# Performance work log

Measured on AMD Instinct MI355X. Metric: run time of the kernel, lower is better.

The kernel has to match this reference:

```python
import jax, jax.numpy as jnp
import numpy as np

D_MODEL = 768
NUM_HEADS = 12
HEAD_DIM = D_MODEL // NUM_HEADS
SEQ = 4096
BATCH = 1


def setup_inputs() -> dict:
    key = jax.random.key(0)
    ks = jax.random.split(key, 6)
    scale = 1.0 / np.sqrt(D_MODEL)
    x = jax.random.normal(ks[0], (BATCH, SEQ, D_MODEL), dtype=jnp.float32)
    mask = jnp.tril(jnp.ones((SEQ, SEQ), dtype=bool))[None, None]  # [1,1,S,S] causal
    Wq = jax.random.normal(ks[1], (D_MODEL, D_MODEL), dtype=jnp.float32) * scale
    Wk = jax.random.normal(ks[2], (D_MODEL, D_MODEL), dtype=jnp.float32) * scale
    Wv = jax.random.normal(ks[3], (D_MODEL, D_MODEL), dtype=jnp.float32) * scale
    Wo = jax.random.normal(ks[4], (D_MODEL, D_MODEL), dtype=jnp.float32) * scale
    bo = jax.random.normal(ks[5], (D_MODEL,), dtype=jnp.float32) * 0.01
    return {"x": x, "mask": mask, "Wq": Wq, "Wk": Wk, "Wv": Wv, "Wo": Wo, "bo": bo}


def _rope_tables(seq_len, head_dim, dtype):
    # inv_freq over even dims; emb = cat(freqs, freqs) but only the first half
    # participates in the well-defined rotation (x1/x2 have head_dim//2 channels)
    inv_freq = 1.0 / (10000.0 ** (jnp.arange(0, head_dim, 2, dtype=dtype) / head_dim))
    t = jnp.arange(seq_len, dtype=dtype)
    freqs = t[:, None] * inv_freq[None, :]  # [S, head_dim//2]
    return jnp.cos(freqs), jnp.sin(freqs)


def _apply_rotary(xh, cos, sin):
    # xh: [B,H,S,hd]; cos/sin: [S, hd//2]
    x1 = xh[..., ::2]
    x2 = xh[..., 1::2]
    # faithful to source: concatenated (not interleaved) rotated halves
    return jnp.concatenate([x1 * cos - x2 * sin, x1 * sin + x2 * cos], axis=-1)


def reference(x, mask, Wq, Wk, Wv, Wo, bo):
    B, S, D = x.shape
    H, hd = NUM_HEADS, HEAD_DIM
    def split_heads(y):
        return y.reshape(B, S, H, hd).transpose(0, 2, 1, 3)  # [B,H,S,hd]
    q = split_heads(x @ Wq.T)
    k = split_heads(x @ Wk.T)
    v = split_heads(x @ Wv.T)
    cos, sin = _rope_tables(S, hd, x.dtype)
    q = _apply_rotary(q, cos, sin)
    k = _apply_rotary(k, cos, sin)
    scores = jnp.einsum('bhqd,bhkd->bhqk', q, k) / jnp.sqrt(jnp.asarray(hd, x.dtype))
    scores = jnp.where(mask, scores, jnp.asarray(-1e9, x.dtype))
    attn = jax.nn.softmax(scores, axis=-1)  # dropout is identity in eval
    out = jnp.einsum('bhqk,bhkd->bhqd', attn, v)
    out = out.transpose(0, 2, 1, 3).reshape(B, S, D)
    return out @ Wo.T + bo
```

## Files before the change

kernel.cpp:

```cpp
#include <hip/hip_runtime.h>
#include <hip/hip_bf16.h>
#include <math.h>

#define SEQ 4096
#define DM  768
#define NH  12
#define HD  64
#define PER ((size_t)NH * SEQ * HD)
#define XN  ((size_t)SEQ * DM)
#define WN  ((size_t)DM * DM)

typedef __attribute__((ext_vector_type(8))) short bf16x8;
typedef __attribute__((ext_vector_type(4))) short s16x4;
typedef __attribute__((ext_vector_type(4))) float f32x4;

#define MFMA(a, b, c) __builtin_amdgcn_mfma_f32_16x16x32_bf16((a), (b), (c), 0, 0, 0)

#if __has_builtin(__builtin_amdgcn_exp2f)
#define EXP2(x) __builtin_amdgcn_exp2f(x)
#else
#define EXP2(x) exp2f(x)
#endif

#define SWZ(row, blk) (((row) << 6) + ((((blk) ^ ((row) & 7))) << 3))

__device__ __forceinline__ unsigned short f2b(float f) {
    unsigned int u = __float_as_uint(f);
    u += 0x7FFFu + ((u >> 16) & 1u);
    return (unsigned short)(u >> 16);
}

__global__ __launch_bounds__(256) void cvt_kernel(const float* __restrict__ src,
                                                  unsigned short* __restrict__ dst,
                                                  int n4) {
    for (int i = blockIdx.x * 256 + threadIdx.x; i < n4; i += gridDim.x * 256) {
        const float4 v = ((const float4*)src)[i];
        s16x4 p;
        p.x = (short)f2b(v.x); p.y = (short)f2b(v.y);
        p.z = (short)f2b(v.z); p.w = (short)f2b(v.w);
        ((s16x4*)dst)[i] = p;
    }
}

__global__ __launch_bounds__(256) void rope_kernel(float2* __restrict__ rope) {
    const int g = blockIdx.x * 256 + threadIdx.x;
    const int row = g >> 5, fi = g & 31;
    const float invf = expf(-(float)fi * 0.28782313662425576f);
    float sn, cs;
    sincosf((float)row * invf, &sn, &cs);
    rope[row * 32 + fi] = make_float2(cs, sn);
}

__global__ __launch_bounds__(256) void qkv_mfma(
    const float* __restrict__ x,  const unsigned short* __restrict__ xb,
    const float* __restrict__ Wq, const float* __restrict__ Wk, const float* __restrict__ Wv,
    const unsigned short* __restrict__ Wqb, const unsigned short* __restrict__ Wkb,
    const unsigned short* __restrict__ Wvb,
    const float2* __restrict__ rope,
    unsigned short* __restrict__ Qo, unsigned short* __restrict__ Ko,
    unsigned short* __restrict__ Vo, int fast)
{
    __shared__ __align__(16) unsigned short Xs[2][4096];
    __shared__ __align__(16) unsigned short Ws[2][4096];
    __shared__ unsigned short VL[64 * 66];

    const int t    = threadIdx.x;
    const int w    = t >> 6;
    const int lane = t & 63;
    const int quad = lane >> 4;
    const int l16  = lane & 15;

    const int nt_b = blockIdx.y;
    const float* W; const unsigned short* Wb; int region;
    if (nt_b < 12)      { W = Wq; Wb = Wqb; region = 0; }
    else if (nt_b < 24) { W = Wk; Wb = Wkb; region = 1; }
    else                { W = Wv; Wb = Wvb; region = 2; }
    const int h  = nt_b % 12;
    const int s0 = blockIdx.x * 64;
    const int n0 = h * 64;

    f32x4 acc[4] = {{0,0,0,0},{0,0,0,0},{0,0,0,0},{0,0,0,0}};
    const int prow = t >> 3, pblk = t & 7;

    bf16x8 xr0, xr1, wr0, wr1;
    if (fast) {
        xr0 = *(const bf16x8*)&xb[(size_t)(s0 + prow) * DM + pblk * 8];
        xr1 = *(const bf16x8*)&xb[(size_t)(s0 + prow + 32) * DM + pblk * 8];
        wr0 = *(const bf16x8*)&Wb[(size_t)(n0 + prow) * DM + pblk * 8];
        wr1 = *(const bf16x8*)&Wb[(size_t)(n0 + prow + 32) * DM + pblk * 8];
        *(bf16x8*)&Xs[0][SWZ(prow, pblk)]      = xr0;
        *(bf16x8*)&Xs[0][SWZ(prow + 32, pblk)] = xr1;
        *(bf16x8*)&Ws[0][SWZ(prow, pblk)]      = wr0;
        *(bf16x8*)&Ws[0][SWZ(prow + 32, pblk)] = wr1;
    } else {
        for (int e = t; e < 1024; e += 256) {
            const int row = e >> 4, c4 = e & 15;
            const int off = SWZ(row, c4 >> 1) + (c4 & 1) * 4;
            const float4 xv = *(const float4*)&x[(size_t)(s0 + row) * DM + c4 * 4];
            s16x4 px; px.x = (short)f2b(xv.x); px.y = (short)f2b(xv.y);
            px.z = (short)f2b(xv.z); px.w = (short)f2b(xv.w);
            *(s16x4*)&Xs[0][off] = px;
            const float4 wv = *(const float4*)&W[(size_t)(n0 + row) * DM + c4 * 4];
            s16x4 pw; pw.x = (short)f2b(wv.x); pw.y = (short)f2b(wv.y);
            pw.z = (short)f2b(wv.z); pw.w = (short)f2b(wv.w);
            *(s16x4*)&Ws[0][off] = pw;
        }
    }
    __syncthreads();

    for (int kt = 0; kt < 12; ++kt) {
        const unsigned short* Xb  = Xs[kt & 1];
        const unsigned short* Wbt = Ws[kt & 1];
        if (fast && kt < 11) {
            const int k0 = (kt + 1) * 64;
            xr0 = *(const bf16x8*)&xb[(size_t)(s0 + prow) * DM + k0 + pblk * 8];
            xr1 = *(const bf16x8*)&xb[(size_t)(s0 + prow + 32) * DM + k0 + pblk * 8];
            wr0 = *(const bf16x8*)&Wb[(size_t)(n0 + prow) * DM + k0 + pblk * 8];
            wr1 = *(const bf16x8*)&Wb[(size_t)(n0 + prow + 32) * DM + k0 + pblk * 8];
        }
        const bf16x8 a0 = *(const bf16x8*)&Xb[SWZ(16 * w + l16, quad)];
        const bf16x8 a1 = *(const bf16x8*)&Xb[SWZ(16 * w + l16, 4 + quad)];
        #pragma unroll
        for (int nt = 0; nt < 4; ++nt) {
            const bf16x8 b0 = *(const bf16x8*)&Wbt[SWZ(16 * nt + l16, quad)];
            const bf16x8 b1 = *(const bf16x8*)&Wbt[SWZ(16 * nt + l16, 4 + quad)];
            acc[nt] = MFMA(a0, b0, acc[nt]);
            acc[nt] = MFMA(a1, b1, acc[nt]);
        }
        if (kt < 11) {
            const int nb = (kt + 1) & 1;
            if (fast) {
                *(bf16x8*)&Xs[nb][SWZ(prow, pblk)]      = xr0;
                *(bf16x8*)&Xs[nb][SWZ(prow + 32, pblk)] = xr1;
                *(bf16x8*)&Ws[nb][SWZ(prow, pblk)]      = wr0;
                *(bf16x8*)&Ws[nb][SWZ(prow + 32, pblk)] = wr1;
            } else {
                const int k0 = (kt + 1) * 64;
                for (int e = t; e < 1024; e += 256) {
                    const int row = e >> 4, c4 = e & 15;
                    const int off = SWZ(row, c4 >> 1) + (c4 & 1) * 4;
                    const float4 xv = *(const float4*)&x[(size_t)(s0 + row) * DM + k0 + c4 * 4];
                    s16x4 px; px.x = (short)f2b(xv.x); px.y = (short)f2b(xv.y);
                    px.z = (short)f2b(xv.z); px.w = (short)f2b(xv.w);
                    *(s16x4*)&Xs[nb][off] = px;
                    const float4 wv = *(const float4*)&W[(size_t)(n0 + row) * DM + k0 + c4 * 4];
                    s16x4 pw; pw.x = (short)f2b(wv.x); pw.y = (short)f2b(wv.y);
                    pw.z = (short)f2b(wv.z); pw.w = (short)f2b(wv.w);
                    *(s16x4*)&Ws[nb][off] = pw;
                }
            }
        }
        __syncthreads();
    }

    const size_t headoff = (size_t)h * SEQ * HD;
    if (region <= 1) {
        unsigned short* dst = (region == 0) ? Qo : Ko;
        const float qsc = (region == 0) ? 0.18033688011112042f : 1.0f;
        #pragma unroll
        for (int nt = 0; nt < 4; ++nt)
            #pragma unroll
            for (int r = 0; r < 4; ++r) {
                const int srow = s0 + 16 * w + quad * 4 + r;
                const int d  = nt * 16 + l16;
                const int fi = d >> 1;
                const float own = acc[nt][r] * qsc;
                const float oth = __shfl_xor(own, 1);
                float cs, sn;
                if (fast) {
                    const float2 t2 = rope[srow * 32 + fi];
                    cs = t2.x; sn = t2.y;
                } else {
                    const float invf = expf(-(float)fi * 0.28782313662425576f);
                    sincosf((float)srow * invf, &sn, &cs);
                }
                const float val = (d & 1) ? (oth * sn + own * cs)
                                          : (own * cs - oth * sn);
                dst[headoff + (size_t)srow * HD + ((d & 1) ? 32 : 0) + fi] = f2b(val);
            }
    } else {
        #pragma unroll
        for (int nt = 0; nt < 4; ++nt)
            #pragma unroll
            for (int r = 0; r < 4; ++r)
                VL[(nt * 16 + l16) * 66 + 16 * w + quad * 4 + r] = f2b(acc[nt][r]);
        __syncthreads();
        for (int e = t; e < 2048; e += 256) {
            const int d = e >> 5, sp = e & 31;
            const unsigned int v = (unsigned int)VL[d * 66 + 2 * sp] |
                                   ((unsigned int)VL[d * 66 + 2 * sp + 1] << 16);
            *(unsigned int*)&Vo[headoff + (size_t)d * SEQ + s0 + 2 * sp] = v;
        }
    }
}

__global__ __launch_bounds__(256) void attn_mfma(
    const unsigned short* __restrict__ Q,
    const unsigned short* __restrict__ K,
    const unsigned short* __restrict__ V,
    unsigned short* __restrict__ O)
{
    __shared__ unsigned short Kst[2][4096];
    __shared__ unsigned short Vt [2][4096];
    __shared__ unsigned short Ps [4096];

    const int h    = blockIdx.y;
    const int q0   = (63 - blockIdx.x) * 64;
    const int t    = threadIdx.x;
    const int w    = t >> 6;
    const int lane = t & 63;
    const int quad = lane >> 4;
    const int l16  = lane & 15;
    const size_t headoff = (size_t)h * SEQ * HD;

    for (int e = t; e < 512; e += 256) {
        const int row = e >> 3, blk = e & 7;
        *(bf16x8*)&Ps[SWZ(row, blk)] =
            *(const bf16x8*)&Q[headoff + (size_t)(q0 + row) * HD + blk * 8];
    }
    const int prow = t >> 3, pblk = t & 7;
    bf16x8 kr0 = *(const bf16x8*)&K[headoff + (size_t)prow * HD + pblk * 8];
    bf16x8 kr1 = *(const bf16x8*)&K[headoff + (size_t)(prow + 32) * HD + pblk * 8];
    bf16x8 vr0 = *(const bf16x8*)&V[headoff + (size_t)prow * SEQ + pblk * 8];
    bf16x8 vr1 = *(const bf16x8*)&V[headoff + (size_t)(prow + 32) * SEQ + pblk * 8];
    *(bf16x8*)&Kst[0][SWZ(prow, pblk)]      = kr0;
    *(bf16x8*)&Kst[0][SWZ(prow + 32, pblk)] = kr1;
    *(bf16x8*)&Vt[0][SWZ(prow, pblk)]       = vr0;
    *(bf16x8*)&Vt[0][SWZ(prow + 32, pblk)]  = vr1;
    __syncthreads();

    const bf16x8 aQ0 = *(const bf16x8*)&Ps[SWZ(16 * w + l16, quad)];
    const bf16x8 aQ1 = *(const bf16x8*)&Ps[SWZ(16 * w + l16, 4 + quad)];

    bf16x8 ones;
    #pragma unroll
    for (int i = 0; i < 8; ++i) ones[i] = (short)0x3F80;

    f32x4 oA[4] = {{0,0,0,0},{0,0,0,0},{0,0,0,0},{0,0,0,0}};
    f32x4 lA = {0, 0, 0, 0};
    const int cmax = q0 >> 6;

    for (int c = 0; c <= cmax; ++c) {
        const unsigned short* Kb = Kst[c & 1];
        const unsigned short* Vb = Vt[c & 1];
        if (c < cmax) {
            const int kn = (c + 1) * 64;
            kr0 = *(const bf16x8*)&K[headoff + (size_t)(kn + prow) * HD + pblk * 8];
            kr1 = *(const bf16x8*)&K[headoff + (size_t)(kn + prow + 32) * HD + pblk * 8];
            vr0 = *(const bf16x8*)&V[headoff + (size_t)prow * SEQ + kn + pblk * 8];
            vr1 = *(const bf16x8*)&V[headoff + (size_t)(prow + 32) * SEQ + kn + pblk * 8];
        }

        f32x4 sA[4] = {{0,0,0,0},{0,0,0,0},{0,0,0,0},{0,0,0,0}};
        #pragma unroll
        for (int nt = 0; nt < 4; ++nt) {
            const bf16x8 b0 = *(const bf16x8*)&Kb[SWZ(16 * nt + l16, quad)];
            const bf16x8 b1 = *(const bf16x8*)&Kb[SWZ(16 * nt + l16, 4 + quad)];
            sA[nt] = MFMA(aQ0, b0, sA[nt]);
            sA[nt] = MFMA(aQ1, b1, sA[nt]);
        }

        if (c == cmax) {
            #pragma unroll
            for (int nt = 0; nt < 4; ++nt) {
                const int key = nt * 16 + l16;
                #pragma unroll
                for (int r = 0; r < 4; ++r) {
                    const int qrel = 16 * w + quad * 4 + r;
                    if (key > qrel) sA[nt][r] = -1e30f;
                }
            }
        }

        #pragma unroll
        for (int nt = 0; nt < 4; ++nt)
            #pragma unroll
            for (int r = 0; r < 4; ++r)
                Ps[SWZ(16 * w + quad * 4 + r, 2 * nt + (l16 >> 3)) + (l16 & 7)] =
                    f2b(EXP2(sA[nt][r]));
        asm volatile("s_waitcnt lgkmcnt(0)" ::: "memory");
        const bf16x8 aP0 = *(const bf16x8*)&Ps[SWZ(16 * w + l16, quad)];
        const bf16x8 aP1 = *(const bf16x8*)&Ps[SWZ(16 * w + l16, 4 + quad)];

        #pragma unroll
        for (int nt = 0; nt < 4; ++nt) {
            const bf16x8 v0 = *(const bf16x8*)&Vb[SWZ(16 * nt + l16, quad)];
            const bf16x8 v1 = *(const bf16x8*)&Vb[SWZ(16 * nt + l16, 4 + quad)];
            oA[nt] = MFMA(aP0, v0, oA[nt]);
            oA[nt] = MFMA(aP1, v1, oA[nt]);
        }
        lA = MFMA(aP0, ones, lA);
        lA = MFMA(aP1, ones, lA);

        if (c < cmax) {
            const int nb = (c + 1) & 1;
            *(bf16x8*)&Kst[nb][SWZ(prow, pblk)]      = kr0;
            *(bf16x8*)&Kst[nb][SWZ(prow + 32, pblk)] = kr1;
            *(bf16x8*)&Vt[nb][SWZ(prow, pblk)]       = vr0;
            *(bf16x8*)&Vt[nb][SWZ(prow + 32, pblk)]  = vr1;
        }
        __syncthreads();
    }

    float inv[4];
    #pragma unroll
    for (int r = 0; r < 4; ++r) inv[r] = 1.0f / lA[r];
    #pragma unroll
    for (int nt = 0; nt < 4; ++nt)
        #pragma unroll
        for (int r = 0; r < 4; ++r) {
            const int q = q0 + 16 * w + quad * 4 + r;
            O[(size_t)q * DM + h * HD + nt * 16 + l16] = f2b(oA[nt][r] * inv[r]);
        }
}

__global__ __launch_bounds__(256) void proj_mfma(
    const unsigned short* __restrict__ A,
    const float* __restrict__ Wo, const unsigned short* __restrict__ Wob,
    const float* __restrict__ bo,
    float* __restrict__ out, int fast)
{
    __shared__ __align__(16) unsigned short Xs[2][4096];
    __shared__ __align__(16) unsigned short Ws[2][4096];

    const int t    = threadIdx.x;
    const int w    = t >> 6;
    const int lane = t & 63;
    const int quad = lane >> 4;
    const int l16  = lane & 15;
    const int s0 = blockIdx.x * 64;
    const int n0 = blockIdx.y * 64;
    const int prow = t >> 3, pblk = t & 7;

    f32x4 acc[4] = {{0,0,0,0},{0,0,0,0},{0,0,0,0},{0,0,0,0}};

    bf16x8 ar0, ar1, wr0, wr1;
    ar0 = *(const bf16x8*)&A[(size_t)(s0 + prow) * DM + pblk * 8];
    ar1 = *(const bf16x8*)&A[(size_t)(s0 + prow + 32) * DM + pblk * 8];
    *(bf16x8*)&Xs[0][SWZ(prow, pblk)]      = ar0;
    *(bf16x8*)&Xs[0][SWZ(prow + 32, pblk)] = ar1;
    if (fast) {
        wr0 = *(const bf16x8*)&Wob[(size_t)(n0 + prow) * DM + pblk * 8];
        wr1 = *(const bf16x8*)&Wob[(size_t)(n0 + prow + 32) * DM + pblk * 8];
        *(bf16x8*)&Ws[0][SWZ(prow, pblk)]      = wr0;
        *(bf16x8*)&Ws[0][SWZ(prow + 32, pblk)] = wr1;
    } else {
        for (int e = t; e < 1024; e += 256) {
            const int row = e >> 4, c4 = e & 15;
            const float4 wv = *(const float4*)&Wo[(size_t)(n0 + row) * DM + c4 * 4];
            s16x4 pw; pw.x = (short)f2b(wv.x); pw.y = (short)f2b(wv.y);
            pw.z = (short)f2b(wv.z); pw.w = (short)f2b(wv.w);
            *(s16x4*)&Ws[0][SWZ(row, c4 >> 1) + (c4 & 1) * 4] = pw;
        }
    }
    __syncthreads();

    for (int kt = 0; kt < 12; ++kt) {
        const unsigned short* Xb  = Xs[kt & 1];
        const unsigned short* Wbt = Ws[kt & 1];
        if (kt < 11) {
            const int k0 = (kt + 1) * 64;
            ar0 = *(const bf16x8*)&A[(size_t)(s0 + prow) * DM + k0 + pblk * 8];
            ar1 = *(const bf16x8*)&A[(size_t)(s0 + prow + 32) * DM + k0 + pblk * 8];
            if (fast) {
                wr0 = *(const bf16x8*)&Wob[(size_t)(n0 + prow) * DM + k0 + pblk * 8];
                wr1 = *(const bf16x8*)&Wob[(size_t)(n0 + prow + 32) * DM + k0 + pblk * 8];
            }
        }
        const bf16x8 a0 = *(const bf16x8*)&Xb[SWZ(16 * w + l16, quad)];
        const bf16x8 a1 = *(const bf16x8*)&Xb[SWZ(16 * w + l16, 4 + quad)];
        #pragma unroll
        for (int nt = 0; nt < 4; ++nt) {
            const bf16x8 b0 = *(const bf16x8*)&Wbt[SWZ(16 * nt + l16, quad)];
            const bf16x8 b1 = *(const bf16x8*)&Wbt[SWZ(16 * nt + l16, 4 + quad)];
            acc[nt] = MFMA(a0, b0, acc[nt]);
            acc[nt] = MFMA(a1, b1, acc[nt]);
        }
        if (kt < 11) {
            const int nb = (kt + 1) & 1;
            *(bf16x8*)&Xs[nb][SWZ(prow, pblk)]      = ar0;
            *(bf16x8*)&Xs[nb][SWZ(prow + 32, pblk)] = ar1;
            if (fast) {
                *(bf16x8*)&Ws[nb][SWZ(prow, pblk)]      = wr0;
                *(bf16x8*)&Ws[nb][SWZ(prow + 32, pblk)] = wr1;
            } else {
                const int k0 = (kt + 1) * 64;
                for (int e = t; e < 1024; e += 256) {
                    const int row = e >> 4, c4 = e & 15;
                    const float4 wv = *(const float4*)&Wo[(size_t)(n0 + row) * DM + k0 + c4 * 4];
                    s16x4 pw; pw.x = (short)f2b(wv.x); pw.y = (short)f2b(wv.y);
                    pw.z = (short)f2b(wv.z); pw.w = (short)f2b(wv.w);
                    *(s16x4*)&Ws[nb][SWZ(row, c4 >> 1) + (c4 & 1) * 4] = pw;
                }
            }
        }
        __syncthreads();
    }

    #pragma unroll
    for (int nt = 0; nt < 4; ++nt)
        #pragma unroll
        for (int r = 0; r < 4; ++r) {
            const int srow = s0 + 16 * w + quad * 4 + r;
            const int n    = n0 + nt * 16 + l16;
            out[(size_t)srow * DM + n] = acc[nt][r] + bo[n];
        }
}

extern "C" void kernel_launch(void* const* d_in, const int* in_sizes, int n_in,
                              void* d_out, int out_size, void* d_ws, size_t ws_size,
                              hipStream_t stream) {
    const float* x  = (const float*)d_in[0];
    const float* Wq = (const float*)d_in[2];
    const float* Wk = (const float*)d_in[3];
    const float* Wv = (const float*)d_in[4];
    const float* Wo = (const float*)d_in[5];
    const float* bo = (const float*)d_in[6];
    float* out = (float*)d_out;

    unsigned short* U  = (unsigned short*)d_ws;
    unsigned short* Qw = U;
    unsigned short* Kw = U + PER;
    unsigned short* Vw = U + 2 * PER;
    unsigned short* Ow = U + 3 * PER;
    unsigned short* xb  = U + 4 * PER;
    unsigned short* Wqb = xb + XN;
    unsigned short* Wkb = Wqb + WN;
    unsigned short* Wvb = Wkb + WN;
    unsigned short* Wob = Wvb + WN;
    float2* rope = (float2*)(Wob + WN);
    const size_t need = (char*)(rope + 4096 * 32) - (char*)d_ws;
    const int fast = (ws_size >= need) ? 1 : 0;

    if (fast) {
        cvt_kernel<<<768, 256, 0, stream>>>(x, xb, (int)(XN / 4));
        cvt_kernel<<<576, 256, 0, stream>>>(Wq, Wqb, (int)(WN / 4));
        cvt_kernel<<<576, 256, 0, stream>>>(Wk, Wkb, (int)(WN / 4));
        cvt_kernel<<<576, 256, 0, stream>>>(Wv, Wvb, (int)(WN / 4));
        cvt_kernel<<<576, 256, 0, stream>>>(Wo, Wob, (int)(WN / 4));
        rope_kernel<<<512, 256, 0, stream>>>(rope);
    }
    qkv_mfma<<<dim3(SEQ / 64, 36), 256, 0, stream>>>(
        x, xb, Wq, Wk, Wv, Wqb, Wkb, Wvb, rope, Qw, Kw, Vw, fast);
    attn_mfma<<<dim3(SEQ / 64, NH), 256, 0, stream>>>(Qw, Kw, Vw, Ow);
    proj_mfma<<<dim3(SEQ / 64, DM / 64), 256, 0, stream>>>(Ow, Wo, Wob, bo, out, fast);
}
```

Baseline: 255.2 us.

## Restructure attention to split key blocks across waves and merge launch-time prep kernels

The attention kernel now loads 128-key chunks. Each wave processes a 32-key slice for all 64 queries, with Q held in registers. Partial O and row-sum accumulators are reduced across waves through shared memory at the end, and the causal loop bound becomes coarser. Separately, the five bf16 conversion launches and the rope table launch are merged into one prep kernel to cut launch overhead. The trade-offs are a single-buffered K/V stage with more barriers, higher register pressure (oT is 16 f32x4 per lane), and a serial cross-wave reduction epilogue.

```diff
diff --git a/kernel.cpp b/kernel.cpp
--- a/kernel.cpp
+++ b/kernel.cpp
@@ -30,25 +30,35 @@
     return (unsigned short)(u >> 16);
 }
 
-__global__ __launch_bounds__(256) void cvt_kernel(const float* __restrict__ src,
-                                                  unsigned short* __restrict__ dst,
-                                                  int n4) {
-    for (int i = blockIdx.x * 256 + threadIdx.x; i < n4; i += gridDim.x * 256) {
-        const float4 v = ((const float4*)src)[i];
-        s16x4 p;
-        p.x = (short)f2b(v.x); p.y = (short)f2b(v.y);
-        p.z = (short)f2b(v.z); p.w = (short)f2b(v.w);
-        ((s16x4*)dst)[i] = p;
-    }
-}
-
-__global__ __launch_bounds__(256) void rope_kernel(float2* __restrict__ rope) {
-    const int g = blockIdx.x * 256 + threadIdx.x;
-    const int row = g >> 5, fi = g & 31;
-    const float invf = expf(-(float)fi * 0.28782313662425576f);
-    float sn, cs;
-    sincosf((float)row * invf, &sn, &cs);
-    rope[row * 32 + fi] = make_float2(cs, sn);
+__global__ __launch_bounds__(256) void prep_kernel(
+    const float* __restrict__ x,  const float* __restrict__ wq,
+    const float* __restrict__ wk, const float* __restrict__ wv,
+    const float* __restrict__ wo,
+    unsigned short* __restrict__ dstbase, float2* __restrict__ rope)
+{
+    const float* srcs[5] = {x, wq, wk, wv, wo};
+    const size_t n4s[5]  = {XN / 4, WN / 4, WN / 4, WN / 4, WN / 4};
+    unsigned short* d = dstbase;
+    for (int rg = 0; rg < 5; ++rg) {
+        const float4* s4 = (const float4*)srcs[rg];
+        s16x4* d4 = (s16x4*)d;
+        for (size_t i = (size_t)blockIdx.x * 256 + threadIdx.x; i < n4s[rg];
+             i += (size_t)gridDim.x * 256) {
+            const float4 v = s4[i];
+            s16x4 p;
+            p.x = (short)f2b(v.x); p.y = (short)f2b(v.y);
+            p.z = (short)f2b(v.z); p.w = (short)f2b(v.w);
+            d4[i] = p;
+        }
+        d += n4s[rg] * 4;
+    }
+    for (int g = blockIdx.x * 256 + threadIdx.x; g < 131072; g += gridDim.x * 256) {
+        const int row = g >> 5, fi = g & 31;
+        const float invf = expf(-(float)fi * 0.28782313662425576f);
+        float sn, cs;
+        sincosf((float)row * invf, &sn, &cs);
+        rope[row * 32 + fi] = make_float2(cs, sn);
+    }
 }
 
 __global__ __launch_bounds__(256) void qkv_mfma(
@@ -194,15 +204,19 @@
     }
 }
 
-__global__ __launch_bounds__(256) void attn_mfma(
+__global__ __launch_bounds__(256, 2) void attn_mfma(
     const unsigned short* __restrict__ Q,
     const unsigned short* __restrict__ K,
     const unsigned short* __restrict__ V,
     unsigned short* __restrict__ O)
 {
-    __shared__ unsigned short Kst[2][4096];
-    __shared__ unsigned short Vt [2][4096];
-    __shared__ unsigned short Ps [4096];
+    __shared__ __align__(16) unsigned char SM[53248];
+    unsigned short* Kst = (unsigned short*)SM;
+    unsigned short* Vt  = (unsigned short*)(SM + 16384);
+    unsigned short* Ps  = (unsigned short*)(SM + 32768);
+    float* ACC  = (float*)SM;
+    float* ACC2 = (float*)(SM + 32768);
+    float* Lx   = (float*)(SM + 51200);
 
     const int h    = blockIdx.y;
     const int q0   = (63 - blockIdx.x) * 64;
@@ -214,104 +228,211 @@
     const size_t headoff = (size_t)h * SEQ * HD;
 
     for (int e = t; e < 512; e += 256) {
-        const int row = e >> 3, blk = e & 7;
-        *(bf16x8*)&Ps[SWZ(row, blk)] =
+        const int row = e >> 3, bp = e & 7, blk = bp ^ (row & 7);
+        *(bf16x8*)&Kst[row * 64 + bp * 8] =
             *(const bf16x8*)&Q[headoff + (size_t)(q0 + row) * HD + blk * 8];
     }
-    const int prow = t >> 3, pblk = t & 7;
-    bf16x8 kr0 = *(const bf16x8*)&K[headoff + (size_t)prow * HD + pblk * 8];
-    bf16x8 kr1 = *(const bf16x8*)&K[headoff + (size_t)(prow + 32) * HD + pblk * 8];
-    bf16x8 vr0 = *(const bf16x8*)&V[headoff + (size_t)prow * SEQ + pblk * 8];
-    bf16x8 vr1 = *(const bf16x8*)&V[headoff + (size_t)(prow + 32) * SEQ + pblk * 8];
-    *(bf16x8*)&Kst[0][SWZ(prow, pblk)]      = kr0;
-    *(bf16x8*)&Kst[0][SWZ(prow + 32, pblk)] = kr1;
-    *(bf16x8*)&Vt[0][SWZ(prow, pblk)]       = vr0;
-    *(bf16x8*)&Vt[0][SWZ(prow + 32, pblk)]  = vr1;
-    __syncthreads();
-
-    const bf16x8 aQ0 = *(const bf16x8*)&Ps[SWZ(16 * w + l16, quad)];
-    const bf16x8 aQ1 = *(const bf16x8*)&Ps[SWZ(16 * w + l16, 4 + quad)];
+    __syncthreads();
+    bf16x8 aQ[4][2];
+    #pragma unroll
+    for (int qt = 0; qt < 4; ++qt)
+        #pragma unroll
+        for (int hh = 0; hh < 2; ++hh)
+            aQ[qt][hh] = *(const bf16x8*)&Kst[SWZ(16 * qt + l16, 4 * hh + quad)];
+    __syncthreads();
+
+    bf16x8 kreg[4], vreg[4];
+    #pragma unroll
+    for (int i = 0; i < 4; ++i) {
+        const int e = t + i * 256, row = e >> 3, bp = e & 7, blk = bp ^ (row & 7);
+        kreg[i] = *(const bf16x8*)&K[headoff + (size_t)row * HD + blk * 8];
+    }
+    #pragma unroll
+    for (int i = 0; i < 4; ++i) {
+        const int e = t + i * 256, row = e >> 4, bp = e & 15, blk = bp ^ (row & 15);
+        vreg[i] = *(const bf16x8*)&V[headoff + (size_t)row * SEQ + blk * 8];
+    }
+    #pragma unroll
+    for (int i = 0; i < 4; ++i) {
+        const int e = t + i * 256, row = e >> 3, bp = e & 7;
+        *(bf16x8*)&Kst[row * 64 + bp * 8] = kreg[i];
+    }
+    #pragma unroll
+    for (int i = 0; i < 4; ++i) {
+        const int e = t + i * 256, row = e >> 4, bp = e & 15;
+        *(bf16x8*)&Vt[row * 128 + bp * 8] = vreg[i];
+    }
+    __syncthreads();
 
     bf16x8 ones;
     #pragma unroll
     for (int i = 0; i < 8; ++i) ones[i] = (short)0x3F80;
 
-    f32x4 oA[4] = {{0,0,0,0},{0,0,0,0},{0,0,0,0},{0,0,0,0}};
-    f32x4 lA = {0, 0, 0, 0};
-    const int cmax = q0 >> 6;
+    f32x4 oT[4][4];
+    #pragma unroll
+    for (int dt = 0; dt < 4; ++dt)
+        #pragma unroll
+        for (int qt = 0; qt < 4; ++qt) oT[dt][qt] = (f32x4){0,0,0,0};
+    f32x4 lT[4] = {{0,0,0,0},{0,0,0,0},{0,0,0,0},{0,0,0,0}};
+
+    unsigned short* usp = Ps + w * 2560;
+    const int cmax = (q0 + 63) >> 7;
 
     for (int c = 0; c <= cmax; ++c) {
-        const unsigned short* Kb = Kst[c & 1];
-        const unsigned short* Vb = Vt[c & 1];
+        const int k0 = c * 128;
+
+        f32x4 sC[4][2];
+        #pragma unroll
+        for (int qt = 0; qt < 4; ++qt)
+            #pragma unroll
+            for (int kt = 0; kt < 2; ++kt) sC[qt][kt] = (f32x4){0,0,0,0};
+        #pragma unroll
+        for (int kt = 0; kt < 2; ++kt) {
+            const int krow = 32 * w + 16 * kt + l16;
+            #pragma unroll
+            for (int hh = 0; hh < 2; ++hh) {
+                const bf16x8 bK = *(const bf16x8*)&Kst[SWZ(krow, 4 * hh + quad)];
+                #pragma unroll
+                for (int qt = 0; qt < 4; ++qt)
+                    sC[qt][kt] = MFMA(aQ[qt][hh], bK, sC[qt][kt]);
+            }
+        }
+
         if (c < cmax) {
-            const int kn = (c + 1) * 64;
-            kr0 = *(const bf16x8*)&K[headoff + (size_t)(kn + prow) * HD + pblk * 8];
-            kr1 = *(const bf16x8*)&K[headoff + (size_t)(kn + prow + 32) * HD + pblk * 8];
-            vr0 = *(const bf16x8*)&V[headoff + (size_t)prow * SEQ + kn + pblk * 8];
-            vr1 = *(const bf16x8*)&V[headoff + (size_t)(prow + 32) * SEQ + kn + pblk * 8];
-        }
-
-        f32x4 sA[4] = {{0,0,0,0},{0,0,0,0},{0,0,0,0},{0,0,0,0}};
-        #pragma unroll
-        for (int nt = 0; nt < 4; ++nt) {
-            const bf16x8 b0 = *(const bf16x8*)&Kb[SWZ(16 * nt + l16, quad)];
-            const bf16x8 b1 = *(const bf16x8*)&Kb[SWZ(16 * nt + l16, 4 + quad)];
-            sA[nt] = MFMA(aQ0, b0, sA[nt]);
-            sA[nt] = MFMA(aQ1, b1, sA[nt]);
+            const int kn = k0 + 128;
+            #pragma unroll
+            for (int i = 0; i < 4; ++i) {
+                const int e = t + i * 256, row = e >> 3, bp = e & 7, blk = bp ^ (row & 7);
+                kreg[i] = *(const bf16x8*)&K[headoff + (size_t)(kn + row) * HD + blk * 8];
+            }
+            #pragma unroll
+            for (int i = 0; i < 4; ++i) {
+                const int e = t + i * 256, row = e >> 4, bp = e & 15, blk = bp ^ (row & 15);
+                vreg[i] = *(const bf16x8*)&V[headoff + (size_t)row * SEQ + kn + blk * 8];
+            }
         }
 
         if (c == cmax) {
             #pragma unroll
-            for (int nt = 0; nt < 4; ++nt) {
-                const int key = nt * 16 + l16;
+            for (int kt = 0; kt < 2; ++kt) {
+                const int key = k0 + 32 * w + 16 * kt + l16;
                 #pragma unroll
-                for (int r = 0; r < 4; ++r) {
-                    const int qrel = 16 * w + quad * 4 + r;
-                    if (key > qrel) sA[nt][r] = -1e30f;
-                }
-            }
-        }
-
-        #pragma unroll
-        for (int nt = 0; nt < 4; ++nt)
-            #pragma unroll
-            for (int r = 0; r < 4; ++r)
-                Ps[SWZ(16 * w + quad * 4 + r, 2 * nt + (l16 >> 3)) + (l16 & 7)] =
-                    f2b(EXP2(sA[nt][r]));
+                for (int qt = 0; qt < 4; ++qt)
+                    #pragma unroll
+                    for (int r = 0; r < 4; ++r)
+                        if (key > q0 + 16 * qt + 4 * quad + r) sC[qt][kt][r] = -1e30f;
+            }
+        }
+
+        #pragma unroll
+        for (int qt = 0; qt < 4; ++qt)
+            #pragma unroll
+            for (int kt = 0; kt < 2; ++kt)
+                #pragma unroll
+                for (int r = 0; r < 4; ++r)
+                    usp[(16 * qt + 4 * quad + r) * 40 + 16 * kt + l16] =
+                        f2b(EXP2(sC[qt][kt][r]));
         asm volatile("s_waitcnt lgkmcnt(0)" ::: "memory");
-        const bf16x8 aP0 = *(const bf16x8*)&Ps[SWZ(16 * w + l16, quad)];
-        const bf16x8 aP1 = *(const bf16x8*)&Ps[SWZ(16 * w + l16, 4 + quad)];
-
-        #pragma unroll
-        for (int nt = 0; nt < 4; ++nt) {
-            const bf16x8 v0 = *(const bf16x8*)&Vb[SWZ(16 * nt + l16, quad)];
-            const bf16x8 v1 = *(const bf16x8*)&Vb[SWZ(16 * nt + l16, 4 + quad)];
-            oA[nt] = MFMA(aP0, v0, oA[nt]);
-            oA[nt] = MFMA(aP1, v1, oA[nt]);
-        }
-        lA = MFMA(aP0, ones, lA);
-        lA = MFMA(aP1, ones, lA);
-
+
+        bf16x8 aV[4];
+        #pragma unroll
+        for (int dt = 0; dt < 4; ++dt) {
+            const int row = 16 * dt + l16;
+            aV[dt] = *(const bf16x8*)&Vt[row * 128 + (((4 * w + quad) ^ (row & 15)) << 3)];
+        }
+        #pragma unroll
+        for (int qt = 0; qt < 4; ++qt) {
+            const bf16x8 bP = *(const bf16x8*)&usp[(16 * qt + l16) * 40 + quad * 8];
+            lT[qt] = MFMA(ones, bP, lT[qt]);
+            #pragma unroll
+            for (int dt = 0; dt < 4; ++dt)
+                oT[dt][qt] = MFMA(aV[dt], bP, oT[dt][qt]);
+        }
+
+        __syncthreads();
         if (c < cmax) {
-            const int nb = (c + 1) & 1;
-            *(bf16x8*)&Kst[nb][SWZ(prow, pblk)]      = kr0;
-            *(bf16x8*)&Kst[nb][SWZ(prow + 32, pblk)] = kr1;
-            *(bf16x8*)&Vt[nb][SWZ(prow, pblk)]       = vr0;
-            *(bf16x8*)&Vt[nb][SWZ(prow + 32, pblk)]  = vr1;
+            #pragma unroll
+            for (int i = 0; i < 4; ++i) {
+                const int e = t + i * 256, row = e >> 3, bp = e & 7;
+                *(bf16x8*)&Kst[row * 64 + bp * 8] = kreg[i];
+            }
+            #pragma unroll
+            for (int i = 0; i < 4; ++i) {
+                const int e = t + i * 256, row = e >> 4, bp = e & 15;
+                *(bf16x8*)&Vt[row * 128 + bp * 8] = vreg[i];
+            }
         }
         __syncthreads();
     }
 
-    float inv[4];
-    #pragma unroll
-    for (int r = 0; r < 4; ++r) inv[r] = 1.0f / lA[r];
-    #pragma unroll
-    for (int nt = 0; nt < 4; ++nt)
-        #pragma unroll
-        for (int r = 0; r < 4; ++r) {
-            const int q = q0 + 16 * w + quad * 4 + r;
-            O[(size_t)q * DM + h * HD + nt * 16 + l16] = f2b(oA[nt][r] * inv[r]);
-        }
+    if (w != 0 && quad == 0) {
+        #pragma unroll
+        for (int qt = 0; qt < 4; ++qt)
+            Lx[w * 64 + 16 * qt + l16] = lT[qt][0];
+    }
+    if (w == 1) {
+        #pragma unroll
+        for (int dt = 0; dt < 4; ++dt)
+            #pragma unroll
+            for (int qt = 0; qt < 4; ++qt)
+                *(f32x4*)&ACC[(16 * qt + l16) * 72 + 16 * dt + 4 * quad] = oT[dt][qt];
+    }
+    __syncthreads();
+    if (w == 0) {
+        #pragma unroll
+        for (int dt = 0; dt < 4; ++dt)
+            #pragma unroll
+            for (int qt = 0; qt < 4; ++qt)
+                oT[dt][qt] += *(const f32x4*)&ACC[(16 * qt + l16) * 72 + 16 * dt + 4 * quad];
+    }
+    if (w == 2) {
+        #pragma unroll
+        for (int dt = 0; dt < 4; ++dt)
+            #pragma unroll
+            for (int qt = 0; qt < 4; ++qt)
+                *(f32x4*)&ACC2[(16 * qt + l16) * 72 + 16 * dt + 4 * quad] = oT[dt][qt];
+    }
+    __syncthreads();
+    if (w == 0) {
+        #pragma unroll
+        for (int dt = 0; dt < 4; ++dt)
+            #pragma unroll
+            for (int qt = 0; qt < 4; ++qt)
+                oT[dt][qt] += *(const f32x4*)&ACC2[(16 * qt + l16) * 72 + 16 * dt + 4 * quad];
+    }
+    if (w == 3) {
+        #pragma unroll
+        for (int dt = 0; dt < 4; ++dt)
+            #pragma unroll
+            for (int qt = 0; qt < 4; ++qt)
+                *(f32x4*)&ACC[(16 * qt + l16) * 72 + 16 * dt + 4 * quad] = oT[dt][qt];
+    }
+    __syncthreads();
+    if (w == 0) {
+        float inv[4];
+        #pragma unroll
+        for (int qt = 0; qt < 4; ++qt) {
+            #pragma unroll
+            for (int dt = 0; dt < 4; ++dt)
+                oT[dt][qt] += *(const f32x4*)&ACC[(16 * qt + l16) * 72 + 16 * dt + 4 * quad];
+            const float ls = lT[qt][0] + Lx[64 + 16 * qt + l16] +
+                             Lx[128 + 16 * qt + l16] + Lx[192 + 16 * qt + l16];
+            inv[qt] = 1.0f / ls;
+        }
+        #pragma unroll
+        for (int qt = 0; qt < 4; ++qt) {
+            const size_t rowoff = (size_t)(q0 + 16 * qt + l16) * DM + h * HD;
+            #pragma unroll
+            for (int dt = 0; dt < 4; ++dt) {
+                ushort4 u;
+                u.x = f2b(oT[dt][qt][0] * inv[qt]);
+                u.y = f2b(oT[dt][qt][1] * inv[qt]);
+                u.z = f2b(oT[dt][qt][2] * inv[qt]);
+                u.w = f2b(oT[dt][qt][3] * inv[qt]);
+                *(ushort4*)&O[rowoff + 16 * dt + 4 * quad] = u;
+            }
+        }
+    }
 }
 
 __global__ __launch_bounds__(256) void proj_mfma(
@@ -432,14 +553,8 @@
     const size_t need = (char*)(rope + 4096 * 32) - (char*)d_ws;
     const int fast = (ws_size >= need) ? 1 : 0;
 
-    if (fast) {
-        cvt_kernel<<<768, 256, 0, stream>>>(x, xb, (int)(XN / 4));
-        cvt_kernel<<<576, 256, 0, stream>>>(Wq, Wqb, (int)(WN / 4));
-        cvt_kernel<<<576, 256, 0, stream>>>(Wk, Wkb, (int)(WN / 4));
-        cvt_kernel<<<576, 256, 0, stream>>>(Wv, Wvb, (int)(WN / 4));
-        cvt_kernel<<<576, 256, 0, stream>>>(Wo, Wob, (int)(WN / 4));
-        rope_kernel<<<512, 256, 0, stream>>>(rope);
-    }
+    if (fast)
+        prep_kernel<<<1024, 256, 0, stream>>>(x, Wq, Wk, Wv, Wo, xb, rope);
     qkv_mfma<<<dim3(SEQ / 64, 36), 256, 0, stream>>>(
         x, xb, Wq, Wk, Wv, Wqb, Wkb, Wvb, rope, Qw, Kw, Vw, fast);
     attn_mfma<<<dim3(SEQ / 64, NH), 256, 0, stream>>>(Qw, Kw, Vw, Ow);
```

Measured after the change: 248.8 us. -2.5%, faster.
